# Kernel tuning notes

Measured on AMD Instinct MI355X. Metric: run time of the kernel, lower is better.

Reference implementation:

```python
import jax, jax.numpy as jnp
import numpy as np

NS, NC = 4, 3
DIAG = 4.1  # 4 + mass (mass = 0.1)
LAT = (16, 16, 16, 16)  # T, Z, Y, X


def setup_inputs() -> dict:
    key = jax.random.key(0)
    ks = jax.random.split(key, 6)
    psi_shape = LAT + (NS, NC)
    K_shape = (4,) + LAT + (NS * NC, NS * NC)
    return {
        "psi_re": jax.random.normal(ks[0], psi_shape, dtype=jnp.float32),
        "psi_im": jax.random.normal(ks[1], psi_shape, dtype=jnp.float32),
        "K_fwd_re": jax.random.normal(ks[2], K_shape, dtype=jnp.float32),
        "K_fwd_im": jax.random.normal(ks[3], K_shape, dtype=jnp.float32),
        "K_bwd_re": jax.random.normal(ks[4], K_shape, dtype=jnp.float32),
        "K_bwd_im": jax.random.normal(ks[5], K_shape, dtype=jnp.float32),
    }


def reference(psi_re, psi_im, K_fwd_re, K_fwd_im, K_bwd_re, K_bwd_im):
    # Flatten spin-color: (T,Z,Y,X,ns,nc) -> (T,Z,Y,X,ns*nc)
    pr = psi_re.reshape(psi_re.shape[:-2] + (NS * NC,))
    pi = psi_im.reshape(psi_im.shape[:-2] + (NS * NC,))
    out_re = DIAG * pr
    out_im = DIAG * pi
    for mu in range(4):
        ldim = mu - 5  # T,Z,Y,X axes of pr (which has 5 dims)
        Kfr, Kfi = K_fwd_re[mu], K_fwd_im[mu]
        Kbr, Kbi = K_bwd_re[mu], K_bwd_im[mu]
        pf_re = jnp.roll(pr, -1, axis=ldim)
        pf_im = jnp.roll(pi, -1, axis=ldim)
        pb_re = jnp.roll(pr, 1, axis=ldim)
        pb_im = jnp.roll(pi, 1, axis=ldim)
        # Complex 12x12 matvec per site: (K_re + i K_im) @ (p_re + i p_im)
        cf_re = jnp.einsum('...ij,...j->...i', Kfr, pf_re) - jnp.einsum('...ij,...j->...i', Kfi, pf_im)
        cf_im = jnp.einsum('...ij,...j->...i', Kfr, pf_im) + jnp.einsum('...ij,...j->...i', Kfi, pf_re)
        cb_re = jnp.einsum('...ij,...j->...i', Kbr, pb_re) - jnp.einsum('...ij,...j->...i', Kbi, pb_im)
        cb_im = jnp.einsum('...ij,...j->...i', Kbr, pb_im) + jnp.einsum('...ij,...j->...i', Kbi, pb_re)
        out_re = out_re - 0.5 * (cf_re + cb_re)
        out_im = out_im - 0.5 * (cf_im + cb_im)
    out_re = out_re.reshape(out_re.shape[:-1] + (NS, NC))
    out_im = out_im.reshape(out_im.shape[:-1] + (NS, NC))
    return (out_re, out_im)
```

## Files before the change

kernel.cpp:

```cpp
#include <hip/hip_runtime.h>

#define VOL   65536
#define NSC   12
#define DIAG  4.1f
#define SPB   16
#define THREADS 192
#define MATF  (SPB * 144)
#define STGF  (2 * MATF)
#define PSI_LINE 192
#define PSI_F (7 * 2 * PSI_LINE)

#define CMADD(kr, ki, vr, vi)                                              \
    sr += kr.x * vr.x - ki.x * vi.x;  si += kr.x * vi.x + ki.x * vr.x;     \
    sr += kr.y * vr.y - ki.y * vi.y;  si += kr.y * vi.y + ki.y * vr.y;     \
    sr += kr.z * vr.z - ki.z * vi.z;  si += kr.z * vi.z + ki.z * vr.z;     \
    sr += kr.w * vr.w - ki.w * vi.w;  si += kr.w * vi.w + ki.w * vr.w;

__device__ __forceinline__ void g2lds16(const float* g, float* l) {
    __builtin_amdgcn_global_load_lds(
        (const __attribute__((address_space(1))) unsigned int*)g,
        (__attribute__((address_space(3))) unsigned int*)l,
        16, 0, 0);
}

template<int P>
__device__ __forceinline__ void stage(const float* Kf_re, const float* Kf_im,
                                      const float* Kb_re, const float* Kb_im,
                                      int site0, int w, int l, float* kb) {
    constexpr int mu = P >> 1;
    const float* re = (P & 1) ? Kb_re : Kf_re;
    const float* im = (P & 1) ? Kb_im : Kf_im;
    const size_t gb = ((size_t)mu * VOL + (size_t)site0) * 144;
    #pragma unroll
    for (int jj = 0; jj < 3; ++jj) {
        const int c = jj * 3 + w;
        g2lds16(re + gb + c * 256 + l * 4, kb + 0 * MATF + c * 256 + l * 4);
        g2lds16(im + gb + c * 256 + l * 4, kb + 1 * MATF + c * 256 + l * 4);
    }
}

template<int P>
__device__ __forceinline__ void phase_compute(const float* kb, const float* pb,
                                              int sl, int j,
                                              float& acc_re, float& acc_im) {
    constexpr int mu = P >> 1;
    constexpr int d  = P & 1;
    constexpr int line = (mu < 3) ? (1 + mu * 2 + d) : 0;
    const int sidx = (mu < 3) ? sl : (d == 0 ? (sl + 1) & 15 : (sl + 15) & 15);

    const float4* kr = (const float4*)(kb + j * 12);
    const float4* ki = (const float4*)(kb + MATF + j * 12);
    const float4* vr = (const float4*)(pb + (line * 2 + 0) * PSI_LINE + sidx * 12);
    const float4* vi = (const float4*)(pb + (line * 2 + 1) * PSI_LINE + sidx * 12);

    float sr = 0.f, si = 0.f;
    #pragma unroll
    for (int q = 0; q < 3; ++q) {
        const float4 a = kr[q], b = ki[q];
        const float4 x = vr[q], y4 = vi[q];
        CMADD(a, b, x, y4);
    }
    acc_re -= 0.5f * sr;
    acc_im -= 0.5f * si;
}

#define WAITV(n) asm volatile("s_waitcnt vmcnt(" #n ")" ::: "memory")
#define CFENCE() asm volatile("" ::: "memory")

__global__ __launch_bounds__(THREADS) void dslash_kernel(
    const float* __restrict__ psi_re, const float* __restrict__ psi_im,
    const float* __restrict__ Kf_re,  const float* __restrict__ Kf_im,
    const float* __restrict__ Kb_re,  const float* __restrict__ Kb_im,
    float* __restrict__ out_re,       float* __restrict__ out_im)
{
    __shared__ float kbuf[2][STGF];
    __shared__ float pbuf[PSI_F];

    const int j  = threadIdx.x;
    const int w  = j >> 6;
    const int l  = j & 63;
    const int sl = j / NSC;
    const int lid = blockIdx.x;
    const int site0 = lid * SPB;

    const int y = lid & 15, z = (lid >> 4) & 15, t = (lid >> 8) & 15;

    int lb[7];
    lb[0] = lid * 192;
    lb[1] = ((((t + 1)  & 15) << 8) | (z << 4) | y) * 192;
    lb[2] = ((((t + 15) & 15) << 8) | (z << 4) | y) * 192;
    lb[3] = ((t << 8) | (((z + 1)  & 15) << 4) | y) * 192;
    lb[4] = ((t << 8) | (((z + 15) & 15) << 4) | y) * 192;
    lb[5] = ((t << 8) | (z << 4) | ((y + 1)  & 15)) * 192;
    lb[6] = ((t << 8) | (z << 4) | ((y + 15) & 15)) * 192;

    #pragma unroll
    for (int r = 0; r < 4; ++r) {
        const int idx = j + r * THREADS;
        if (idx < 672) {
            const int c  = idx % 48;
            const int la = idx / 48;
            const int ar = la & 1, ln = la >> 1;
            const float4 v = *(const float4*)((ar ? psi_im : psi_re) + lb[ln] + c * 4);
            *(float4*)&pbuf[(ln * 2 + ar) * PSI_LINE + c * 4] = v;
        }
    }
    __syncthreads();

    float acc_re = DIAG * pbuf[0 * PSI_LINE + j];
    float acc_im = DIAG * pbuf[1 * PSI_LINE + j];

    stage<0>(Kf_re, Kf_im, Kb_re, Kb_im, site0, w, l, kbuf[0]);
    stage<1>(Kf_re, Kf_im, Kb_re, Kb_im, site0, w, l, kbuf[1]);

#define DO_PHASE(P, NWAIT)                                                    \
    WAITV(NWAIT);                                                             \
    __builtin_amdgcn_s_barrier();                                             \
    CFENCE();                                                                 \
    phase_compute<P>(kbuf[(P) & 1], pbuf, sl, j, acc_re, acc_im);             \
    CFENCE();                                                                 \
    __builtin_amdgcn_s_barrier();                                             \
    CFENCE();

    DO_PHASE(0, 6)
    stage<2>(Kf_re, Kf_im, Kb_re, Kb_im, site0, w, l, kbuf[0]);
    DO_PHASE(1, 6)
    stage<3>(Kf_re, Kf_im, Kb_re, Kb_im, site0, w, l, kbuf[1]);
    DO_PHASE(2, 6)
    stage<4>(Kf_re, Kf_im, Kb_re, Kb_im, site0, w, l, kbuf[0]);
    DO_PHASE(3, 6)
    stage<5>(Kf_re, Kf_im, Kb_re, Kb_im, site0, w, l, kbuf[1]);
    DO_PHASE(4, 6)
    stage<6>(Kf_re, Kf_im, Kb_re, Kb_im, site0, w, l, kbuf[0]);
    DO_PHASE(5, 6)
    stage<7>(Kf_re, Kf_im, Kb_re, Kb_im, site0, w, l, kbuf[1]);
    DO_PHASE(6, 6)
    DO_PHASE(7, 0)

    out_re[site0 * NSC + j] = acc_re;
    out_im[site0 * NSC + j] = acc_im;
}

extern "C" void kernel_launch(void* const* d_in, const int* in_sizes, int n_in,
                              void* d_out, int out_size, void* d_ws, size_t ws_size,
                              hipStream_t stream) {
    const float* psi_re = (const float*)d_in[0];
    const float* psi_im = (const float*)d_in[1];
    const float* Kf_re  = (const float*)d_in[2];
    const float* Kf_im  = (const float*)d_in[3];
    const float* Kb_re  = (const float*)d_in[4];
    const float* Kb_im  = (const float*)d_in[5];

    float* out_re = (float*)d_out;
    float* out_im = (float*)d_out + (size_t)VOL * NSC;

    dslash_kernel<<<VOL / SPB, THREADS, 0, stream>>>(psi_re, psi_im,
                                                     Kf_re, Kf_im, Kb_re, Kb_im,
                                                     out_re, out_im);
}
```

Before: 113.7 us.

## Give each wavefront its own K row slice to drop block barriers in pipeline

Each wavefront now stages only the 4 matrix rows it computes (row block w of each site) into a private LDS slice, so the per-phase double-buffered pipeline needs only vmcnt/lgkmcnt waits instead of two block-wide barriers per phase. The psi buffer is re-laid out as float4 planes indexed by site to avoid bank conflicts, and the thread-to-(site,row) mapping changes accordingly. Global loads for K become more scattered, with 48-byte contiguous chunks per site-row instead of fully linear lines, which may lower coalescing efficiency in exchange for less synchronization.

```diff
diff --git a/kernel.cpp b/kernel.cpp
--- a/kernel.cpp
+++ b/kernel.cpp
@@ -5,10 +5,8 @@
 #define DIAG  4.1f
 #define SPB   16
 #define THREADS 192
-#define MATF  (SPB * 144)
-#define STGF  (2 * MATF)
-#define PSI_LINE 192
-#define PSI_F (7 * 2 * PSI_LINE)
+#define KWF   1536
+#define PQ(line, ar, q) (((line)*2 + (ar))*3 + (q))
 
 #define CMADD(kr, ki, vr, vi)                                              \
     sr += kr.x * vr.x - ki.x * vi.x;  si += kr.x * vi.x + ki.x * vr.x;     \
@@ -23,49 +21,55 @@
         16, 0, 0);
 }
 
+#define WAITV(n) asm volatile("s_waitcnt vmcnt(" #n ")" ::: "memory")
+#define WAITL()  asm volatile("s_waitcnt lgkmcnt(0)" ::: "memory")
+#define SBAR()   __builtin_amdgcn_sched_barrier(0)
+
 template<int P>
-__device__ __forceinline__ void stage(const float* Kf_re, const float* Kf_im,
-                                      const float* Kb_re, const float* Kb_im,
-                                      int site0, int w, int l, float* kb) {
+__device__ __forceinline__ void stageK(const float* __restrict__ Kf_re,
+                                       const float* __restrict__ Kf_im,
+                                       const float* __restrict__ Kb_re,
+                                       const float* __restrict__ Kb_im,
+                                       int site0, int w, int l,
+                                       const int* goff, float* kwb) {
     constexpr int mu = P >> 1;
     const float* re = (P & 1) ? Kb_re : Kf_re;
     const float* im = (P & 1) ? Kb_im : Kf_im;
-    const size_t gb = ((size_t)mu * VOL + (size_t)site0) * 144;
+    const size_t gb = ((size_t)(mu * VOL) + (size_t)site0) * 36 + (size_t)w * 12;
     #pragma unroll
     for (int jj = 0; jj < 3; ++jj) {
-        const int c = jj * 3 + w;
-        g2lds16(re + gb + c * 256 + l * 4, kb + 0 * MATF + c * 256 + l * 4);
-        g2lds16(im + gb + c * 256 + l * 4, kb + 1 * MATF + c * 256 + l * 4);
+        const size_t g4 = gb + (size_t)goff[jj];
+        g2lds16(re + 4 * g4, kwb + 0 * 768 + jj * 256 + l * 4);
+        g2lds16(im + 4 * g4, kwb + 1 * 768 + jj * 256 + l * 4);
     }
 }
 
 template<int P>
-__device__ __forceinline__ void phase_compute(const float* kb, const float* pb,
-                                              int sl, int j,
+__device__ __forceinline__ void phase_compute(const float* __restrict__ kwb,
+                                              const float* __restrict__ pbuf,
+                                              int s, int r,
                                               float& acc_re, float& acc_im) {
     constexpr int mu = P >> 1;
     constexpr int d  = P & 1;
     constexpr int line = (mu < 3) ? (1 + mu * 2 + d) : 0;
-    const int sidx = (mu < 3) ? sl : (d == 0 ? (sl + 1) & 15 : (sl + 15) & 15);
+    const int sidx = (mu < 3) ? s : (d == 0 ? (s + 1) & 15 : (s + 15) & 15);
 
-    const float4* kr = (const float4*)(kb + j * 12);
-    const float4* ki = (const float4*)(kb + MATF + j * 12);
-    const float4* vr = (const float4*)(pb + (line * 2 + 0) * PSI_LINE + sidx * 12);
-    const float4* vi = (const float4*)(pb + (line * 2 + 1) * PSI_LINE + sidx * 12);
+    const float4* k4 = (const float4*)kwb;
+    const float4* p4 = (const float4*)pbuf;
+    const int kb = s * 12 + r * 3;
 
     float sr = 0.f, si = 0.f;
     #pragma unroll
     for (int q = 0; q < 3; ++q) {
-        const float4 a = kr[q], b = ki[q];
-        const float4 x = vr[q], y4 = vi[q];
+        const float4 a = k4[kb + q];
+        const float4 b = k4[192 + kb + q];
+        const float4 x = p4[PQ(line, 0, q) * 16 + sidx];
+        const float4 y4 = p4[PQ(line, 1, q) * 16 + sidx];
         CMADD(a, b, x, y4);
     }
     acc_re -= 0.5f * sr;
     acc_im -= 0.5f * si;
 }
-
-#define WAITV(n) asm volatile("s_waitcnt vmcnt(" #n ")" ::: "memory")
-#define CFENCE() asm volatile("" ::: "memory")
 
 __global__ __launch_bounds__(THREADS) void dslash_kernel(
     const float* __restrict__ psi_re, const float* __restrict__ psi_im,
@@ -73,17 +77,25 @@
     const float* __restrict__ Kb_re,  const float* __restrict__ Kb_im,
     float* __restrict__ out_re,       float* __restrict__ out_im)
 {
-    __shared__ float kbuf[2][STGF];
-    __shared__ float pbuf[PSI_F];
+    __shared__ float kbuf[3][2][KWF];
+    __shared__ float pbuf[672 * 4];
 
     const int j  = threadIdx.x;
     const int w  = j >> 6;
     const int l  = j & 63;
-    const int sl = j / NSC;
+    const int s  = l >> 2;
+    const int r  = l & 3;
     const int lid = blockIdx.x;
     const int site0 = lid * SPB;
+    const int y = lid & 15, z = (lid >> 4) & 15, t = (lid >> 8) & 15;
 
-    const int y = lid & 15, z = (lid >> 4) & 15, t = (lid >> 8) & 15;
+    int goff[3];
+    #pragma unroll
+    for (int jj = 0; jj < 3; ++jj) {
+        const int c = jj * 64 + l;
+        const int ss = c / 12;
+        goff[jj] = ss * 36 + (c - ss * 12);
+    }
 
     int lb[7];
     lb[0] = lid * 192;
@@ -95,50 +107,49 @@
     lb[6] = ((t << 8) | (z << 4) | ((y + 15) & 15)) * 192;
 
     #pragma unroll
-    for (int r = 0; r < 4; ++r) {
-        const int idx = j + r * THREADS;
+    for (int rr = 0; rr < 4; ++rr) {
+        const int idx = j + rr * THREADS;
         if (idx < 672) {
             const int c  = idx % 48;
             const int la = idx / 48;
             const int ar = la & 1, ln = la >> 1;
             const float4 v = *(const float4*)((ar ? psi_im : psi_re) + lb[ln] + c * 4);
-            *(float4*)&pbuf[(ln * 2 + ar) * PSI_LINE + c * 4] = v;
+            const int q = c % 3, st = c / 3;
+            *(float4*)&pbuf[(PQ(ln, ar, q) * 16 + st) * 4] = v;
         }
     }
-    __syncthreads();
+    SBAR();
 
-    float acc_re = DIAG * pbuf[0 * PSI_LINE + j];
-    float acc_im = DIAG * pbuf[1 * PSI_LINE + j];
+    float* kwb0 = &kbuf[w][0][0];
+    float* kwb1 = &kbuf[w][1][0];
+    stageK<0>(Kf_re, Kf_im, Kb_re, Kb_im, site0, w, l, goff, kwb0);
+    stageK<1>(Kf_re, Kf_im, Kb_re, Kb_im, site0, w, l, goff, kwb1);
+    SBAR();
+    WAITL();
+    __builtin_amdgcn_s_barrier();
 
-    stage<0>(Kf_re, Kf_im, Kb_re, Kb_im, site0, w, l, kbuf[0]);
-    stage<1>(Kf_re, Kf_im, Kb_re, Kb_im, site0, w, l, kbuf[1]);
+    float acc_re = DIAG * pbuf[PQ(0, 0, w) * 64 + l];
+    float acc_im = DIAG * pbuf[PQ(0, 1, w) * 64 + l];
 
-#define DO_PHASE(P, NWAIT)                                                    \
-    WAITV(NWAIT);                                                             \
-    __builtin_amdgcn_s_barrier();                                             \
-    CFENCE();                                                                 \
-    phase_compute<P>(kbuf[(P) & 1], pbuf, sl, j, acc_re, acc_im);             \
-    CFENCE();                                                                 \
-    __builtin_amdgcn_s_barrier();                                             \
-    CFENCE();
+#define PHASE(P, NW)                                                          \
+    WAITV(NW);                                                                \
+    SBAR();                                                                   \
+    phase_compute<P>(((P) & 1) ? kwb1 : kwb0, pbuf, s, r, acc_re, acc_im);    \
+    WAITL();    \
+    SBAR();
 
-    DO_PHASE(0, 6)
-    stage<2>(Kf_re, Kf_im, Kb_re, Kb_im, site0, w, l, kbuf[0]);
-    DO_PHASE(1, 6)
-    stage<3>(Kf_re, Kf_im, Kb_re, Kb_im, site0, w, l, kbuf[1]);
-    DO_PHASE(2, 6)
-    stage<4>(Kf_re, Kf_im, Kb_re, Kb_im, site0, w, l, kbuf[0]);
-    DO_PHASE(3, 6)
-    stage<5>(Kf_re, Kf_im, Kb_re, Kb_im, site0, w, l, kbuf[1]);
-    DO_PHASE(4, 6)
-    stage<6>(Kf_re, Kf_im, Kb_re, Kb_im, site0, w, l, kbuf[0]);
-    DO_PHASE(5, 6)
-    stage<7>(Kf_re, Kf_im, Kb_re, Kb_im, site0, w, l, kbuf[1]);
-    DO_PHASE(6, 6)
-    DO_PHASE(7, 0)
+    PHASE(0, 6) stageK<2>(Kf_re, Kf_im, Kb_re, Kb_im, site0, w, l, goff, kwb0);
+    PHASE(1, 6) stageK<3>(Kf_re, Kf_im, Kb_re, Kb_im, site0, w, l, goff, kwb1);
+    PHASE(2, 6) stageK<4>(Kf_re, Kf_im, Kb_re, Kb_im, site0, w, l, goff, kwb0);
+    PHASE(3, 6) stageK<5>(Kf_re, Kf_im, Kb_re, Kb_im, site0, w, l, goff, kwb1);
+    PHASE(4, 6) stageK<6>(Kf_re, Kf_im, Kb_re, Kb_im, site0, w, l, goff, kwb0);
+    PHASE(5, 6) stageK<7>(Kf_re, Kf_im, Kb_re, Kb_im, site0, w, l, goff, kwb1);
+    PHASE(6, 6)
+    PHASE(7, 0)
 
-    out_re[site0 * NSC + j] = acc_re;
-    out_im[site0 * NSC + j] = acc_im;
+    const int o = (site0 + s) * NSC + 4 * w + r;
+    out_re[o] = acc_re;
+    out_im[o] = acc_im;
 }
 
 extern "C" void kernel_launch(void* const* d_in, const int* in_sizes, int n_in,
```

After: 113.6 us. About the same (-0.1%).
